# Performance work log

Measured on AMD Instinct MI355X. Metric: run time of the kernel, lower is better.

Reference implementation:

```python
import jax, jax.numpy as jnp
import numpy as np


def setup_inputs() -> dict:
    key = jax.random.key(0)
    k1, k2 = jax.random.split(key)
    N, D, O, K = 65536, 256, 256, 8  # tokens, inputdim, outdim, degree+1
    gridsize = 8
    x = jax.random.normal(k1, (N, D), dtype=jnp.float32)
    # init stddev = 1/(sqrt(inputdim)*sqrt(gridsize)) as in the module
    std = 1.0 / (np.sqrt(D) * np.sqrt(gridsize))
    cheby_coeffs = jax.random.normal(k2, (O, D, K), dtype=jnp.float32) * std
    bias = jnp.zeros((1, O), dtype=jnp.float32)
    return {"x": x, "cheby_coeffs": cheby_coeffs, "bias": bias}


def reference(x, cheby_coeffs, bias):
    # x: (N, D); cheby_coeffs: (O, D, K); bias: (1, O)
    K = cheby_coeffs.shape[-1]
    xt = jnp.tanh(x)                       # squash into [-1, 1]
    theta = jnp.arccos(xt)                 # (N, D)
    n = jnp.arange(K, dtype=x.dtype)       # Chebyshev orders 0..degree
    # T_n(xt) = cos(n * arccos(xt)), matching the original per-degree loop
    T = jnp.cos(theta[..., None] * n)      # (N, D, K)
    y = jnp.einsum('ndk,odk->no', T, cheby_coeffs)  # (N, O)
    y = y + bias
    return y
```

## Files before the change

### kernel.cpp

```cpp
#include <hip/hip_runtime.h>
#include <hip/hip_bf16.h>

typedef __attribute__((ext_vector_type(4)))  int   i32x4;
typedef __attribute__((ext_vector_type(16))) int   i32x16;

#define DIM_D 256
#define DIM_O 256
#define DIM_K 8
#define BM 128
#define NCHUNK 16
#define NSTEP 4
#define MAGIC 12582912.f

__global__ __launch_bounds__(256) void pack_w_kernel(
    const float* __restrict__ coeffs,
    unsigned int* __restrict__ wp,
    float* __restrict__ scales)
{
    const int o = blockIdx.x;
    const int d = threadIdx.x;
    const float* cp = coeffs + ((size_t)o * DIM_D + d) * DIM_K;
    float4 c0 = *(const float4*)cp;
    float4 c1 = *(const float4*)(cp + 4);

    float m = fmaxf(fmaxf(fmaxf(fabsf(c0.x), fabsf(c0.y)),
                          fmaxf(fabsf(c0.z), fabsf(c0.w))),
                    fmaxf(fmaxf(fabsf(c1.x), fabsf(c1.y)),
                          fmaxf(fabsf(c1.z), fabsf(c1.w))));
    #pragma unroll
    for (int i = 32; i >= 1; i >>= 1)
        m = fmaxf(m, __shfl_xor(m, i));
    __shared__ float wm[4];
    if ((d & 63) == 0) wm[d >> 6] = m;
    __syncthreads();
    const float sc = fmaxf(fmaxf(fmaxf(wm[0], wm[1]), fmaxf(wm[2], wm[3])),
                           1e-30f);
    if (d == 0) scales[o] = sc;

    const float inv = 127.0f / sc;
    unsigned f0 = __float_as_uint(__builtin_fmaf(c0.x, inv, MAGIC));
    unsigned f1 = __float_as_uint(__builtin_fmaf(c0.y, inv, MAGIC));
    unsigned f2 = __float_as_uint(__builtin_fmaf(c0.z, inv, MAGIC));
    unsigned f3 = __float_as_uint(__builtin_fmaf(c0.w, inv, MAGIC));
    unsigned f4 = __float_as_uint(__builtin_fmaf(c1.x, inv, MAGIC));
    unsigned f5 = __float_as_uint(__builtin_fmaf(c1.y, inv, MAGIC));
    unsigned f6 = __float_as_uint(__builtin_fmaf(c1.z, inv, MAGIC));
    unsigned f7 = __float_as_uint(__builtin_fmaf(c1.w, inv, MAGIC));
    unsigned rA = __builtin_amdgcn_perm(f1, f0, 0x00000400u);
    unsigned rB = __builtin_amdgcn_perm(f3, f2, 0x00000400u);
    unsigned rC = __builtin_amdgcn_perm(f5, f4, 0x00000400u);
    unsigned rD = __builtin_amdgcn_perm(f7, f6, 0x00000400u);
    unsigned lo = __builtin_amdgcn_perm(rB, rA, 0x05040100u);
    unsigned hi = __builtin_amdgcn_perm(rD, rC, 0x05040100u);

    const int base = (((d >> 2) * 8 + (o >> 5)) * 64
                      + ((d >> 1) & 1) * 32 + (o & 31)) * 4 + (d & 1) * 2;
    wp[base]     = lo;
    wp[base + 1] = hi;
}

__device__ __forceinline__ void cheb_q8(float xs, unsigned int* o2) {
    float e2 = __expf(2.f * xs);
    float r  = __builtin_amdgcn_rcpf(e2 + 1.f);
    float T1 = __builtin_fmaf(-2.f, r, 1.f);
    float tx = T1 + T1;
    float T2 = __builtin_fmaf(tx, T1, -1.f);
    float T3 = __builtin_fmaf(tx, T2, -T1);
    float T4 = __builtin_fmaf(tx, T3, -T2);
    float T5 = __builtin_fmaf(tx, T4, -T3);
    float T6 = __builtin_fmaf(tx, T5, -T4);
    float T7 = __builtin_fmaf(tx, T6, -T5);
    unsigned f1 = __float_as_uint(__builtin_fmaf(T1, 127.f, MAGIC));
    unsigned f2 = __float_as_uint(__builtin_fmaf(T2, 127.f, MAGIC));
    unsigned f3 = __float_as_uint(__builtin_fmaf(T3, 127.f, MAGIC));
    unsigned f4 = __float_as_uint(__builtin_fmaf(T4, 127.f, MAGIC));
    unsigned f5 = __float_as_uint(__builtin_fmaf(T5, 127.f, MAGIC));
    unsigned f6 = __float_as_uint(__builtin_fmaf(T6, 127.f, MAGIC));
    unsigned f7 = __float_as_uint(__builtin_fmaf(T7, 127.f, MAGIC));
    unsigned rA = __builtin_amdgcn_perm(f2, f1, 0x00000400u);
    unsigned rC = __builtin_amdgcn_perm(f5, f4, 0x00000400u);
    unsigned rD = __builtin_amdgcn_perm(f7, f6, 0x00000400u);
    o2[0] = __builtin_amdgcn_perm(f3, rA, 0x0401000Cu) | 127u;
    o2[1] = __builtin_amdgcn_perm(rD, rC, 0x05040100u);
}

__global__ __launch_bounds__(256, 2) void cfkan_kernel(
    const float* __restrict__ x,
    const i32x4* __restrict__ wp8,
    const float* __restrict__ scales,
    const float* __restrict__ bias,
    float* __restrict__ y)
{
    __shared__ unsigned char Abuf[2][BM][128];

    const int t = threadIdx.x;
    const int w = t >> 6;
    const int l = t & 63;
    const int m = l & 31;
    const int h = l >> 5;
    const int row0 = blockIdx.x * BM;

    i32x16 acc[4][2];
    #pragma unroll
    for (int rt = 0; rt < 4; ++rt)
        #pragma unroll
        for (int ct = 0; ct < 2; ++ct)
            #pragma unroll
            for (int q = 0; q < 16; ++q)
                acc[rt][ct][q] = 0;

    const int lrow = t >> 1;
    const int half = t & 1;
    const float* xrow = x + (size_t)(row0 + lrow) * DIM_D + half * 8;

#define READA(DST, AB, S) do {                                             \
    const int _so = (((2 * (S) + h) ^ (m & 7)) * 16);                      \
    DST[0] = *(const i32x4*)&AB[      m][_so];                             \
    DST[1] = *(const i32x4*)&AB[ 32 + m][_so];                             \
    DST[2] = *(const i32x4*)&AB[ 64 + m][_so];                             \
    DST[3] = *(const i32x4*)&AB[ 96 + m][_so];                             \
} while (0)
#define LOADB2(DST, SG) do {                                               \
    DST[0] = wp8[((SG) * 8 + w * 2 + 0) * 64 + l];                         \
    DST[1] = wp8[((SG) * 8 + w * 2 + 1) * 64 + l];                         \
} while (0)
#define STAGE2(ANX, S, X0, X1) do {                                        \
    union { unsigned int u[4]; i32x4 v; } _tv;                             \
    cheb_q8(X0, &_tv.u[0]);                                                \
    cheb_q8(X1, &_tv.u[2]);                                                \
    *(i32x4*)&ANX[lrow][(((half * 4 + (S)) ^ (lrow & 7)) * 16)] = _tv.v;   \
} while (0)
#define SOFT_BARRIER() do {                                                \
    asm volatile("s_waitcnt lgkmcnt(0)" ::: "memory");                     \
    __builtin_amdgcn_s_barrier();                                          \
    __builtin_amdgcn_sched_barrier(0);                                     \
} while (0)

    float xv[8];
    {
        float4 a0 = *(const float4*)xrow;
        float4 a1 = *(const float4*)(xrow + 4);
        float xs[8] = {a0.x, a0.y, a0.z, a0.w, a1.x, a1.y, a1.z, a1.w};
        #pragma unroll
        for (int s = 0; s < 4; ++s)
            STAGE2(Abuf[0], s, xs[2 * s], xs[2 * s + 1]);
        float4 b0 = *(const float4*)(xrow + 16);
        float4 b1 = *(const float4*)(xrow + 16 + 4);
        xv[0] = b0.x; xv[1] = b0.y; xv[2] = b0.z; xv[3] = b0.w;
        xv[4] = b1.x; xv[5] = b1.y; xv[6] = b1.z; xv[7] = b1.w;
    }
    i32x4 bc[2], bn[2];
    LOADB2(bc, 0);
    SOFT_BARRIER();
    i32x4 r[4], rn[4];
    READA(r, Abuf[0], 0);

    #pragma unroll 1
    for (int c = 0; c < NCHUNK; ++c) {
        const unsigned char (*A)[128] = Abuf[c & 1];
        unsigned char (*ANX)[128]     = Abuf[(c & 1) ^ 1];
        const bool stage = (c < NCHUNK - 1);
        float4 xn0, xn1;
        if (c + 2 < NCHUNK) {
            xn0 = *(const float4*)(xrow + (c + 2) * 16);
            xn1 = *(const float4*)(xrow + (c + 2) * 16 + 4);
        }

        #pragma unroll
        for (int s = 0; s < NSTEP; ++s) {
            LOADB2(bn, (c * 4 + s + 1) & 63);
            if (s < NSTEP - 1) READA(rn, A, s + 1);

            __builtin_amdgcn_s_setprio(1);
            #pragma unroll
            for (int rt = 0; rt < 4; ++rt) {
                acc[rt][0] = __builtin_amdgcn_mfma_i32_32x32x32_i8(
                    r[rt], bc[0], acc[rt][0], 0, 0, 0);
                acc[rt][1] = __builtin_amdgcn_mfma_i32_32x32x32_i8(
                    r[rt], bc[1], acc[rt][1], 0, 0, 0);
            }
            __builtin_amdgcn_s_setprio(0);

            if (stage) STAGE2(ANX, s, xv[2 * s], xv[2 * s + 1]);

            if (s < NSTEP - 1) { r[0] = rn[0]; r[1] = rn[1]; r[2] = rn[2]; r[3] = rn[3]; }
            bc[0] = bn[0]; bc[1] = bn[1];
        }
        if (c + 2 < NCHUNK) {
            xv[0] = xn0.x; xv[1] = xn0.y; xv[2] = xn0.z; xv[3] = xn0.w;
            xv[4] = xn1.x; xv[5] = xn1.y; xv[6] = xn1.z; xv[7] = xn1.w;
        }
        SOFT_BARRIER();
        if (c < NCHUNK - 1) READA(r, ANX, 0);
    }

    #pragma unroll
    for (int ct = 0; ct < 2; ++ct) {
        const int col = w * 64 + ct * 32 + m;
        const float sf = scales[col] * (1.f / 16129.f);
        const float bv = bias[col];
        #pragma unroll
        for (int rt = 0; rt < 4; ++rt) {
            #pragma unroll
            for (int q = 0; q < 16; ++q) {
                const int grow = row0 + rt * 32 + (q & 3) + 8 * (q >> 2) + 4 * h;
                y[(size_t)grow * DIM_O + col] =
                    __builtin_fmaf((float)acc[rt][ct][q], sf, bv);
            }
        }
    }
#undef READA
#undef LOADB2
#undef STAGE2
#undef SOFT_BARRIER
}

extern "C" void kernel_launch(void* const* d_in, const int* in_sizes, int n_in,
                              void* d_out, int out_size, void* d_ws, size_t ws_size,
                              hipStream_t stream) {
    const float* x      = (const float*)d_in[0];
    const float* coeffs = (const float*)d_in[1];
    const float* bias   = (const float*)d_in[2];
    float* y = (float*)d_out;
    float*        scales = (float*)d_ws;
    unsigned int* wp     = (unsigned int*)((char*)d_ws + 1024);

    const int n_tokens = in_sizes[0] / DIM_D;

    pack_w_kernel<<<DIM_O, 256, 0, stream>>>(coeffs, wp, scales);
    cfkan_kernel<<<n_tokens / BM, 256, 0, stream>>>(
        x, (const i32x4*)wp, scales, bias, y);
}
```

Baseline: 54.89 us.

## Split 128-row tile across 8 waves in 2x4 grid with 512-thread blocks

Doubles the block to 512 threads so 8 waves share a 128x256 output tile as a 2x4 wave grid, each wave computing 64x64 instead of 128x64. Each thread now stages 4 x values per chunk instead of 8, halving per-thread Chebyshev/quantization work and register use (accumulators drop from 8 to 4 tiles). The aim is more resident waves for latency hiding and more parallel staging. The cost is that each wave reloads the same weight fragments, doubling B global/L2 traffic per block, and MFMA work per wave is smaller relative to barrier overhead.

```diff
diff --git a/kernel.cpp b/kernel.cpp
--- a/kernel.cpp
+++ b/kernel.cpp
@@ -84,7 +84,7 @@
     o2[1] = __builtin_amdgcn_perm(rD, rC, 0x05040100u);
 }
 
-__global__ __launch_bounds__(256, 2) void cfkan_kernel(
+__global__ __launch_bounds__(512, 4) void cfkan_kernel(
     const float* __restrict__ x,
     const i32x4* __restrict__ wp8,
     const float* __restrict__ scales,
@@ -94,41 +94,41 @@
     __shared__ unsigned char Abuf[2][BM][128];
 
     const int t = threadIdx.x;
-    const int w = t >> 6;
+    const int wid = t >> 6;
+    const int wc = wid & 3;
+    const int wr = wid >> 2;
     const int l = t & 63;
     const int m = l & 31;
     const int h = l >> 5;
     const int row0 = blockIdx.x * BM;
 
-    i32x16 acc[4][2];
+    i32x16 acc[2][2];
     #pragma unroll
-    for (int rt = 0; rt < 4; ++rt)
+    for (int rt = 0; rt < 2; ++rt)
         #pragma unroll
         for (int ct = 0; ct < 2; ++ct)
             #pragma unroll
-            for (int q = 0; q < 16; ++q)
-                acc[rt][ct][q] = 0;
-
-    const int lrow = t >> 1;
-    const int half = t & 1;
-    const float* xrow = x + (size_t)(row0 + lrow) * DIM_D + half * 8;
+            for (int qi = 0; qi < 16; ++qi)
+                acc[rt][ct][qi] = 0;
+
+    const int lrow = t >> 2;
+    const int tq   = t & 3;
+    const float* xrow = x + (size_t)(row0 + lrow) * DIM_D + tq * 4;
 
 #define READA(DST, AB, S) do {                                             \
     const int _so = (((2 * (S) + h) ^ (m & 7)) * 16);                      \
-    DST[0] = *(const i32x4*)&AB[      m][_so];                             \
-    DST[1] = *(const i32x4*)&AB[ 32 + m][_so];                             \
-    DST[2] = *(const i32x4*)&AB[ 64 + m][_so];                             \
-    DST[3] = *(const i32x4*)&AB[ 96 + m][_so];                             \
+    DST[0] = *(const i32x4*)&AB[wr * 64 +      m][_so];                    \
+    DST[1] = *(const i32x4*)&AB[wr * 64 + 32 + m][_so];                    \
 } while (0)
 #define LOADB2(DST, SG) do {                                               \
-    DST[0] = wp8[((SG) * 8 + w * 2 + 0) * 64 + l];                         \
-    DST[1] = wp8[((SG) * 8 + w * 2 + 1) * 64 + l];                         \
-} while (0)
-#define STAGE2(ANX, S, X0, X1) do {                                        \
+    DST[0] = wp8[((SG) * 8 + wc * 2 + 0) * 64 + l];                        \
+    DST[1] = wp8[((SG) * 8 + wc * 2 + 1) * 64 + l];                        \
+} while (0)
+#define STAGE2(ANX, J, X0, X1) do {                                        \
     union { unsigned int u[4]; i32x4 v; } _tv;                             \
     cheb_q8(X0, &_tv.u[0]);                                                \
     cheb_q8(X1, &_tv.u[2]);                                                \
-    *(i32x4*)&ANX[lrow][(((half * 4 + (S)) ^ (lrow & 7)) * 16)] = _tv.v;   \
+    *(i32x4*)&ANX[lrow][(((tq * 2 + (J)) ^ (lrow & 7)) * 16)] = _tv.v;     \
 } while (0)
 #define SOFT_BARRIER() do {                                                \
     asm volatile("s_waitcnt lgkmcnt(0)" ::: "memory");                     \
@@ -136,23 +136,16 @@
     __builtin_amdgcn_sched_barrier(0);                                     \
 } while (0)
 
-    float xv[8];
     {
-        float4 a0 = *(const float4*)xrow;
-        float4 a1 = *(const float4*)(xrow + 4);
-        float xs[8] = {a0.x, a0.y, a0.z, a0.w, a1.x, a1.y, a1.z, a1.w};
-        #pragma unroll
-        for (int s = 0; s < 4; ++s)
-            STAGE2(Abuf[0], s, xs[2 * s], xs[2 * s + 1]);
-        float4 b0 = *(const float4*)(xrow + 16);
-        float4 b1 = *(const float4*)(xrow + 16 + 4);
-        xv[0] = b0.x; xv[1] = b0.y; xv[2] = b0.z; xv[3] = b0.w;
-        xv[4] = b1.x; xv[5] = b1.y; xv[6] = b1.z; xv[7] = b1.w;
+        float4 xc = *(const float4*)xrow;
+        STAGE2(Abuf[0], 0, xc.x, xc.y);
+        STAGE2(Abuf[0], 1, xc.z, xc.w);
     }
+    float4 xv = *(const float4*)(xrow + 16);
     i32x4 bc[2], bn[2];
     LOADB2(bc, 0);
     SOFT_BARRIER();
-    i32x4 r[4], rn[4];
+    i32x4 r[2], rn[2];
     READA(r, Abuf[0], 0);
 
     #pragma unroll 1
@@ -160,11 +153,9 @@
         const unsigned char (*A)[128] = Abuf[c & 1];
         unsigned char (*ANX)[128]     = Abuf[(c & 1) ^ 1];
         const bool stage = (c < NCHUNK - 1);
-        float4 xn0, xn1;
-        if (c + 2 < NCHUNK) {
-            xn0 = *(const float4*)(xrow + (c + 2) * 16);
-            xn1 = *(const float4*)(xrow + (c + 2) * 16 + 4);
-        }
+        float4 xn;
+        if (c + 2 < NCHUNK)
+            xn = *(const float4*)(xrow + (c + 2) * 16);
 
         #pragma unroll
         for (int s = 0; s < NSTEP; ++s) {
@@ -172,40 +163,41 @@
             if (s < NSTEP - 1) READA(rn, A, s + 1);
 
             __builtin_amdgcn_s_setprio(1);
-            #pragma unroll
-            for (int rt = 0; rt < 4; ++rt) {
-                acc[rt][0] = __builtin_amdgcn_mfma_i32_32x32x32_i8(
-                    r[rt], bc[0], acc[rt][0], 0, 0, 0);
-                acc[rt][1] = __builtin_amdgcn_mfma_i32_32x32x32_i8(
-                    r[rt], bc[1], acc[rt][1], 0, 0, 0);
-            }
+            acc[0][0] = __builtin_amdgcn_mfma_i32_32x32x32_i8(
+                r[0], bc[0], acc[0][0], 0, 0, 0);
+            acc[0][1] = __builtin_amdgcn_mfma_i32_32x32x32_i8(
+                r[0], bc[1], acc[0][1], 0, 0, 0);
+            acc[1][0] = __builtin_amdgcn_mfma_i32_32x32x32_i8(
+                r[1], bc[0], acc[1][0], 0, 0, 0);
+            acc[1][1] = __builtin_amdgcn_mfma_i32_32x32x32_i8(
+                r[1], bc[1], acc[1][1], 0, 0, 0);
             __builtin_amdgcn_s_setprio(0);
 
-            if (stage) STAGE2(ANX, s, xv[2 * s], xv[2 * s + 1]);
-
-            if (s < NSTEP - 1) { r[0] = rn[0]; r[1] = rn[1]; r[2] = rn[2]; r[3] = rn[3]; }
+            if (s == 1 && stage) STAGE2(ANX, 0, xv.x, xv.y);
+            if (s == 3 && stage) STAGE2(ANX, 1, xv.z, xv.w);
+
+            if (s < NSTEP - 1) { r[0] = rn[0]; r[1] = rn[1]; }
             bc[0] = bn[0]; bc[1] = bn[1];
         }
-        if (c + 2 < NCHUNK) {
-            xv[0] = xn0.x; xv[1] = xn0.y; xv[2] = xn0.z; xv[3] = xn0.w;
-            xv[4] = xn1.x; xv[5] = xn1.y; xv[6] = xn1.z; xv[7] = xn1.w;
-        }
+        if (c + 2 < NCHUNK) xv = xn;
+
         SOFT_BARRIER();
         if (c < NCHUNK - 1) READA(r, ANX, 0);
     }
 
     #pragma unroll
     for (int ct = 0; ct < 2; ++ct) {
-        const int col = w * 64 + ct * 32 + m;
+        const int col = wc * 64 + ct * 32 + m;
         const float sf = scales[col] * (1.f / 16129.f);
         const float bv = bias[col];
         #pragma unroll
-        for (int rt = 0; rt < 4; ++rt) {
+        for (int rt = 0; rt < 2; ++rt) {
             #pragma unroll
-            for (int q = 0; q < 16; ++q) {
-                const int grow = row0 + rt * 32 + (q & 3) + 8 * (q >> 2) + 4 * h;
+            for (int qi = 0; qi < 16; ++qi) {
+                const int grow = row0 + wr * 64 + rt * 32
+                               + (qi & 3) + 8 * (qi >> 2) + 4 * h;
                 y[(size_t)grow * DIM_O + col] =
-                    __builtin_fmaf((float)acc[rt][ct][q], sf, bv);
+                    __builtin_fmaf((float)acc[rt][ct][qi], sf, bv);
             }
         }
     }
@@ -228,6 +220,6 @@
     const int n_tokens = in_sizes[0] / DIM_D;
 
     pack_w_kernel<<<DIM_O, 256, 0, stream>>>(coeffs, wp, scales);
-    cfkan_kernel<<<n_tokens / BM, 256, 0, stream>>>(
+    cfkan_kernel<<<n_tokens / BM, 512, 0, stream>>>(
         x, (const i32x4*)wp, scales, bias, y);
 }
```

New measurement: 56.97 us. 3.8% more time.
